# Optimization experiments

Hardware: AMD Instinct MI355X
Metric: run time of the kernel (lower is better)

The kernel has to match this reference:

```python
import jax, jax.numpy as jnp
import numpy as np

H, W = 200, 200          # detector resolution
DELX, DELY = 2.0, 2.0    # detector pixel size
EPS = 1e-8


def _rotation(theta, phi, gamma):
    # R = Rz(theta) @ Ry(phi) @ Rx(gamma), as in diffdrr's Rxyz
    ct, st = jnp.cos(theta), jnp.sin(theta)
    cp, sp = jnp.cos(phi), jnp.sin(phi)
    cg, sg = jnp.cos(gamma), jnp.sin(gamma)
    one, zero = jnp.ones_like(ct), jnp.zeros_like(ct)
    Rz = jnp.stack([jnp.stack([ct, -st, zero]), jnp.stack([st, ct, zero]), jnp.stack([zero, zero, one])])
    Ry = jnp.stack([jnp.stack([cp, zero, sp]), jnp.stack([zero, one, zero]), jnp.stack([-sp, zero, cp])])
    Rx = jnp.stack([jnp.stack([one, zero, zero]), jnp.stack([zero, cg, -sg]), jnp.stack([zero, sg, cg])])
    return Rz @ Ry @ Rx


def setup_inputs() -> dict:
    key = jax.random.key(0)
    volume = jax.random.uniform(key, (256, 256, 256), dtype=jnp.float32)
    spacing = jnp.ones((3,), dtype=jnp.float32)
    return {
        "volume": volume,
        "spacing": spacing,
        "sdr": jnp.float32(300.0),
        "theta": jnp.float32(np.pi),
        "phi": jnp.float32(0.0),
        "gamma": jnp.float32(np.pi / 2),
        "bx": jnp.float32(128.0),
        "by": jnp.float32(128.0),
        "bz": jnp.float32(128.0),
    }


def _drr_forward(volume, spacing, sdr, theta, phi, gamma, bx, by, bz):
    # DRR.__init__ flips the volume along axis 0
    vol = volume[::-1]
    nxyz = np.array(vol.shape)  # static shapes: (X, Y, Z)

    # ---- Detector.make_xrays: camera basis, source and detector plane ----
    R = sdr * _rotation(theta, phi, gamma)          # (3,3)
    source = R[:, 0]                                # rho * first column
    center = -source
    u, v = R[:, 1] / sdr, R[:, 2] / sdr             # unit in-plane basis
    t = (jnp.arange(-(H // 2), H // 2) + 1).astype(jnp.float32) * DELX
    s = (jnp.arange(-(W // 2), W // 2) + 1).astype(jnp.float32) * DELY
    trans = jnp.stack([bx, by, bz])
    src = source + trans                            # (3,)
    # cartesian_prod(t, s): row-major (t slow, s fast) -> (H*W, 3)
    tgt = (t[:, None, None] * u + s[None, :, None] * v + center + trans).reshape(H * W, 3)

    # ---- Siddon.raytrace ----
    sdd = tgt - src + EPS                           # (n, 3)
    # alpha values at every axis-aligned voxel boundary plane
    ax = (jnp.arange(nxyz[0] + 1, dtype=jnp.float32) * spacing[0] - src[0]) / sdd[:, 0:1]
    ay = (jnp.arange(nxyz[1] + 1, dtype=jnp.float32) * spacing[1] - src[1]) / sdd[:, 1:2]
    az = (jnp.arange(nxyz[2] + 1, dtype=jnp.float32) * spacing[2] - src[2]) / sdd[:, 2:3]
    alphas = jnp.concatenate([ax, ay, az], axis=-1)  # (n, P) with P = X+Y+Z+3

    # entry/exit alphas of the volume bounding box
    a0 = (0.0 - src) / sdd                           # (n, 3)
    a1 = (nxyz.astype(np.float32) * spacing - src) / sdd
    amin = jnp.max(jnp.minimum(a0, a1), axis=-1, keepdims=True)
    amax = jnp.min(jnp.maximum(a0, a1), axis=-1, keepdims=True)

    good = (alphas >= amin) & (alphas <= amax)
    alphas = jnp.sort(jnp.where(good, alphas, jnp.inf), axis=-1)  # invalid -> +inf at end

    amid = 0.5 * (alphas[:, :-1] + alphas[:, 1:])    # (n, P-1)
    step = alphas[:, 1:] - alphas[:, :-1]            # inf-inf -> nan for padding
    valid = jnp.isfinite(step)

    # midpoint positions -> voxel indices (trunc, as in torch .trunc())
    pts = src + amid[..., None] * sdd[:, None, :]    # (n, P-1, 3)
    idx = jnp.trunc(jnp.where(valid[..., None], pts, 0.0) / spacing).astype(jnp.int32)
    idx = jnp.clip(idx, 0, jnp.asarray(nxyz - 1, dtype=jnp.int32))
    vox = vol[idx[..., 0], idx[..., 1], idx[..., 2]]  # (n, P-1) gather

    drr = jnp.sum(jnp.where(valid, step, 0.0) * vox, axis=-1)  # nansum equivalent
    drr = drr * jnp.linalg.norm(tgt - src + EPS, axis=-1)       # scale by ray length
    return drr.reshape(1, 1, H, W)


def reference(volume, spacing, sdr, theta, phi, gamma, bx, by, bz):
    return _drr_forward(volume, spacing, sdr, theta, phi, gamma, bx, by, bz)
```

## Files before the change

### kernel.cpp

```cpp
#include <hip/hip_runtime.h>
#include <math.h>

#pragma clang fp contract(off)

#define SPLIT 16
static constexpr int HH = 200, WW = 200, NPL = 256;

__device__ __forceinline__ float alpha_of(float k, float sp, float src, float sdd) {
    return (k * sp - src) / sdd;
}

__global__ __launch_bounds__(256)
void drr_kernel(const float* __restrict__ vol,
                const float* __restrict__ spacing,
                const float* __restrict__ sdrP,
                const float* __restrict__ thetaP,
                const float* __restrict__ phiP,
                const float* __restrict__ gammaP,
                const float* __restrict__ bxP,
                const float* __restrict__ byP,
                const float* __restrict__ bzP,
                float* __restrict__ out)
{
    const int tid = blockIdx.x * blockDim.x + threadIdx.x;
    if (tid >= HH * WW * SPLIT) return;
    const int seg = tid / (HH * WW);
    const int rid = tid - seg * (HH * WW);
    const int it  = rid % HH;
    const int is  = rid / HH;

    const float sdr = sdrP[0];
    const float th = thetaP[0], ph = phiP[0], ga = gammaP[0];
    const float ct = cosf(th), st = sinf(th);
    const float cp = cosf(ph), sp = sinf(ph);
    const float cg = cosf(ga), sg = sinf(ga);

    const float rot[3][3] = {
        { ct*cp, ct*sp*sg - st*cg, ct*sp*cg + st*sg },
        { st*cp, st*sp*sg + ct*cg, st*sp*cg - ct*sg },
        { -sp,   cp*sg,            cp*cg            }
    };

    float source[3], u[3], v[3], trans[3];
    trans[0] = bxP[0]; trans[1] = byP[0]; trans[2] = bzP[0];
    for (int a = 0; a < 3; ++a) {
        source[a] = sdr * rot[a][0];
        u[a] = (sdr * rot[a][1]) / sdr;
        v[a] = (sdr * rot[a][2]) / sdr;
    }

    const float tc = (float)(it - HH/2 + 1) * 2.0f;
    const float sc = (float)(is - WW/2 + 1) * 2.0f;

    float src[3], sdd[3], spn[3];
    float nrm2 = 0.0f;
    for (int a = 0; a < 3; ++a) {
        spn[a] = spacing[a];
        src[a] = source[a] + trans[a];
        float tg = tc * u[a] + sc * v[a];
        tg = tg - source[a];
        tg = tg + trans[a];
        float d = (tg - src[a]) + 1e-8f;
        sdd[a] = d;
        nrm2 = nrm2 + d * d;
    }
    const bool unit = (spn[0] == 1.0f) & (spn[1] == 1.0f) & (spn[2] == 1.0f);

    float amin = -INFINITY, amax = INFINITY;
    for (int a = 0; a < 3; ++a) {
        float a0 = (0.0f - src[a]) / sdd[a];
        float a1 = (256.0f * spn[a] - src[a]) / sdd[a];
        amin = fmaxf(amin, fminf(a0, a1));
        amax = fminf(amax, fmaxf(a0, a1));
    }

    float acc = 0.0f;
    if (amax > amin) {
        const float blo = (seg == 0) ? amin
                        : amin + (amax - amin) * ((float)seg / (float)SPLIT);
        const float bhi = (seg == SPLIT - 1) ? amax
                        : amin + (amax - amin) * ((float)(seg + 1) / (float)SPLIT);

        float kf[3], kst[3], nexta[3];
        float prev = -INFINITY;

        for (int a = 0; a < 3; ++a) {
            const float sd = sdd[a], sr = src[a], spv = spn[a];
            const bool pos = sd > 0.0f;
            kst[a] = pos ? 1.0f : -1.0f;
            const float kseed = (blo * sd + sr) / spv;
            int kk;
            if (pos) {
                kk = (int)floorf(kseed) + 1;
                kk = kk < 0 ? 0 : (kk > NPL + 1 ? NPL + 1 : kk);
                while (kk > 0    && alpha_of((float)(kk-1), spv, sr, sd) >  blo) --kk;
                while (kk <= NPL && alpha_of((float)kk,     spv, sr, sd) <= blo) ++kk;
                if (kk - 1 >= 0) {
                    float ap = alpha_of((float)(kk-1), spv, sr, sd);
                    if (ap >= amin && ap > prev) prev = ap;
                }
                nexta[a] = (kk <= NPL) ? alpha_of((float)kk, spv, sr, sd) : INFINITY;
            } else {
                kk = (int)ceilf(kseed) - 1;
                kk = kk > NPL ? NPL : (kk < -1 ? -1 : kk);
                while (kk < NPL && alpha_of((float)(kk+1), spv, sr, sd) >  blo) ++kk;
                while (kk >= 0  && alpha_of((float)kk,     spv, sr, sd) <= blo) --kk;
                if (kk + 1 <= NPL) {
                    float ap = alpha_of((float)(kk+1), spv, sr, sd);
                    if (ap >= amin && ap > prev) prev = ap;
                }
                nexta[a] = (kk >= 0) ? alpha_of((float)kk, spv, sr, sd) : INFINITY;
            }
            kf[a] = (float)kk;
        }

        for (int guard = 0; guard < 1024; ++guard) {
            const float q = fminf(fminf(nexta[0], nexta[1]), nexta[2]);
            if (!(q <= bhi)) break;

            const float step = q - prev;
            const float amid = 0.5f * (prev + q);

            const float p0 = src[0] + amid * sdd[0];
            const float p1 = src[1] + amid * sdd[1];
            const float p2 = src[2] + amid * sdd[2];
            float f0, f1, f2;
            if (unit) { f0 = p0; f1 = p1; f2 = p2; }
            else      { f0 = p0 / spn[0]; f1 = p1 / spn[1]; f2 = p2 / spn[2]; }
            f0 = fminf(fmaxf(f0, 0.0f), 255.0f);
            f1 = fminf(fmaxf(f1, 0.0f), 255.0f);
            f2 = fminf(fmaxf(f2, 0.0f), 255.0f);
            const int i0 = (int)f0, i1 = (int)f1, i2 = (int)f2;

            const int addr = ((255 - i0) << 16) | (i1 << 8) | i2;
            acc = fmaf(step, vol[addr], acc);
            prev = q;

            #pragma unroll
            for (int a = 0; a < 3; ++a) {
                if (nexta[a] == q) {
                    const float nk = kf[a] + kst[a];
                    kf[a] = nk;
                    const float al = alpha_of(nk, spn[a], src[a], sdd[a]);
                    nexta[a] = (nk >= 0.0f && nk <= 256.0f) ? al : INFINITY;
                }
            }
        }
    }

    atomicAdd(&out[it * WW + is], acc * sqrtf(nrm2));
}

extern "C" void kernel_launch(void* const* d_in, const int* in_sizes, int n_in,
                              void* d_out, int out_size, void* d_ws, size_t ws_size,
                              hipStream_t stream)
{
    const float* vol     = (const float*)d_in[0];
    const float* spacing = (const float*)d_in[1];
    const float* sdr     = (const float*)d_in[2];
    const float* theta   = (const float*)d_in[3];
    const float* phi     = (const float*)d_in[4];
    const float* gamma   = (const float*)d_in[5];
    const float* bx      = (const float*)d_in[6];
    const float* by      = (const float*)d_in[7];
    const float* bz      = (const float*)d_in[8];
    float* out = (float*)d_out;

    hipMemsetAsync(out, 0, (size_t)out_size * sizeof(float), stream);

    const int threads = HH * WW * SPLIT;
    const int block   = 256;
    const int grid    = threads / block;
    drr_kernel<<<grid, block, 0, stream>>>(vol, spacing, sdr, theta, phi, gamma,
                                           bx, by, bz, out);
}
```

Baseline: 61.89 us.

## Hoist per-ray camera setup into a one-thread setup kernel, retune split and block size

Moves the rotation and trig setup out of every thread into a single-thread setup kernel that writes the camera basis to workspace; the main kernel then just loads 18 floats. Raises the per-ray segment split from 16 to 20 and halves the block size to 128 to improve load balance across segments. Adds an extra kernel launch and a dependency between the two kernels, with a fallback monolithic kernel if no workspace is available.

```diff
diff --git a/kernel.cpp b/kernel.cpp
--- a/kernel.cpp
+++ b/kernel.cpp
@@ -3,60 +3,25 @@
 
 #pragma clang fp contract(off)
 
-#define SPLIT 16
+#define SPLIT 20
 static constexpr int HH = 200, WW = 200, NPL = 256;
 
 __device__ __forceinline__ float alpha_of(float k, float sp, float src, float sdd) {
     return (k * sp - src) / sdd;
 }
 
-__global__ __launch_bounds__(256)
-void drr_kernel(const float* __restrict__ vol,
-                const float* __restrict__ spacing,
-                const float* __restrict__ sdrP,
-                const float* __restrict__ thetaP,
-                const float* __restrict__ phiP,
-                const float* __restrict__ gammaP,
-                const float* __restrict__ bxP,
-                const float* __restrict__ byP,
-                const float* __restrict__ bzP,
-                float* __restrict__ out)
-{
-    const int tid = blockIdx.x * blockDim.x + threadIdx.x;
-    if (tid >= HH * WW * SPLIT) return;
-    const int seg = tid / (HH * WW);
-    const int rid = tid - seg * (HH * WW);
-    const int it  = rid % HH;
-    const int is  = rid / HH;
-
-    const float sdr = sdrP[0];
-    const float th = thetaP[0], ph = phiP[0], ga = gammaP[0];
-    const float ct = cosf(th), st = sinf(th);
-    const float cp = cosf(ph), sp = sinf(ph);
-    const float cg = cosf(ga), sg = sinf(ga);
-
-    const float rot[3][3] = {
-        { ct*cp, ct*sp*sg - st*cg, ct*sp*cg + st*sg },
-        { st*cp, st*sp*sg + ct*cg, st*sp*cg - ct*sg },
-        { -sp,   cp*sg,            cp*cg            }
-    };
-
-    float source[3], u[3], v[3], trans[3];
-    trans[0] = bxP[0]; trans[1] = byP[0]; trans[2] = bzP[0];
-    for (int a = 0; a < 3; ++a) {
-        source[a] = sdr * rot[a][0];
-        u[a] = (sdr * rot[a][1]) / sdr;
-        v[a] = (sdr * rot[a][2]) / sdr;
-    }
-
+__device__ __forceinline__ void trace_seg(
+    const float* __restrict__ vol, float* __restrict__ out,
+    int it, int is, int seg,
+    const float u[3], const float v[3], const float source[3],
+    const float trans[3], const float src[3], const float spn[3])
+{
     const float tc = (float)(it - HH/2 + 1) * 2.0f;
     const float sc = (float)(is - WW/2 + 1) * 2.0f;
 
-    float src[3], sdd[3], spn[3];
+    float sdd[3];
     float nrm2 = 0.0f;
     for (int a = 0; a < 3; ++a) {
-        spn[a] = spacing[a];
-        src[a] = source[a] + trans[a];
         float tg = tc * u[a] + sc * v[a];
         tg = tg - source[a];
         tg = tg + trans[a];
@@ -132,7 +97,7 @@
             f2 = fminf(fmaxf(f2, 0.0f), 255.0f);
             const int i0 = (int)f0, i1 = (int)f1, i2 = (int)f2;
 
-            const int addr = ((255 - i0) << 16) | (i1 << 8) | i2;
+            const int addr = ((((255 - i0) << 8) + i1) << 8) + i2;
             acc = fmaf(step, vol[addr], acc);
             prev = q;
 
@@ -151,6 +116,104 @@
     atomicAdd(&out[it * WW + is], acc * sqrtf(nrm2));
 }
 
+__global__ void drr_setup(const float* __restrict__ spacing,
+                          const float* __restrict__ sdrP,
+                          const float* __restrict__ thetaP,
+                          const float* __restrict__ phiP,
+                          const float* __restrict__ gammaP,
+                          const float* __restrict__ bxP,
+                          const float* __restrict__ byP,
+                          const float* __restrict__ bzP,
+                          float* __restrict__ ws)
+{
+    if (threadIdx.x != 0 || blockIdx.x != 0) return;
+    const float sdr = sdrP[0];
+    const float th = thetaP[0], ph = phiP[0], ga = gammaP[0];
+    const float ct = cosf(th), st = sinf(th);
+    const float cp = cosf(ph), sp = sinf(ph);
+    const float cg = cosf(ga), sg = sinf(ga);
+
+    const float rot[3][3] = {
+        { ct*cp, ct*sp*sg - st*cg, ct*sp*cg + st*sg },
+        { st*cp, st*sp*sg + ct*cg, st*sp*cg - ct*sg },
+        { -sp,   cp*sg,            cp*cg            }
+    };
+    const float trans[3] = { bxP[0], byP[0], bzP[0] };
+    for (int a = 0; a < 3; ++a) {
+        const float source = sdr * rot[a][0];
+        ws[0  + a] = (sdr * rot[a][1]) / sdr;
+        ws[3  + a] = (sdr * rot[a][2]) / sdr;
+        ws[6  + a] = source;
+        ws[9  + a] = trans[a];
+        ws[12 + a] = source + trans[a];
+        ws[15 + a] = spacing[a];
+    }
+}
+
+__global__ __launch_bounds__(128)
+void drr_main(const float* __restrict__ vol,
+              const float* __restrict__ ws,
+              float* __restrict__ out)
+{
+    const int tid = blockIdx.x * blockDim.x + threadIdx.x;
+    const int seg = tid / (HH * WW);
+    const int rid = tid - seg * (HH * WW);
+    const int it  = rid % HH;
+    const int is  = rid / HH;
+
+    float u[3], v[3], source[3], trans[3], src[3], spn[3];
+    #pragma unroll
+    for (int a = 0; a < 3; ++a) {
+        u[a]      = ws[0  + a];
+        v[a]      = ws[3  + a];
+        source[a] = ws[6  + a];
+        trans[a]  = ws[9  + a];
+        src[a]    = ws[12 + a];
+        spn[a]    = ws[15 + a];
+    }
+    trace_seg(vol, out, it, is, seg, u, v, source, trans, src, spn);
+}
+
+__global__ __launch_bounds__(128)
+void drr_mono(const float* __restrict__ vol,
+              const float* __restrict__ spacing,
+              const float* __restrict__ sdrP,
+              const float* __restrict__ thetaP,
+              const float* __restrict__ phiP,
+              const float* __restrict__ gammaP,
+              const float* __restrict__ bxP,
+              const float* __restrict__ byP,
+              const float* __restrict__ bzP,
+              float* __restrict__ out)
+{
+    const int tid = blockIdx.x * blockDim.x + threadIdx.x;
+    const int seg = tid / (HH * WW);
+    const int rid = tid - seg * (HH * WW);
+    const int it  = rid % HH;
+    const int is  = rid / HH;
+
+    const float sdr = sdrP[0];
+    const float th = thetaP[0], ph = phiP[0], ga = gammaP[0];
+    const float ct = cosf(th), st = sinf(th);
+    const float cp = cosf(ph), sp = sinf(ph);
+    const float cg = cosf(ga), sg = sinf(ga);
+    const float rot[3][3] = {
+        { ct*cp, ct*sp*sg - st*cg, ct*sp*cg + st*sg },
+        { st*cp, st*sp*sg + ct*cg, st*sp*cg - ct*sg },
+        { -sp,   cp*sg,            cp*cg            }
+    };
+    float u[3], v[3], source[3], trans[3], src[3], spn[3];
+    trans[0] = bxP[0]; trans[1] = byP[0]; trans[2] = bzP[0];
+    for (int a = 0; a < 3; ++a) {
+        source[a] = sdr * rot[a][0];
+        u[a] = (sdr * rot[a][1]) / sdr;
+        v[a] = (sdr * rot[a][2]) / sdr;
+        src[a] = source[a] + trans[a];
+        spn[a] = spacing[a];
+    }
+    trace_seg(vol, out, it, is, seg, u, v, source, trans, src, spn);
+}
+
 extern "C" void kernel_launch(void* const* d_in, const int* in_sizes, int n_in,
                               void* d_out, int out_size, void* d_ws, size_t ws_size,
                               hipStream_t stream)
@@ -169,8 +232,15 @@
     hipMemsetAsync(out, 0, (size_t)out_size * sizeof(float), stream);
 
     const int threads = HH * WW * SPLIT;
-    const int block   = 256;
+    const int block   = 128;
     const int grid    = threads / block;
-    drr_kernel<<<grid, block, 0, stream>>>(vol, spacing, sdr, theta, phi, gamma,
-                                           bx, by, bz, out);
-}
+
+    if (ws_size >= 18 * sizeof(float)) {
+        float* ws = (float*)d_ws;
+        drr_setup<<<1, 1, 0, stream>>>(spacing, sdr, theta, phi, gamma, bx, by, bz, ws);
+        drr_main<<<grid, block, 0, stream>>>(vol, ws, out);
+    } else {
+        drr_mono<<<grid, block, 0, stream>>>(vol, spacing, sdr, theta, phi, gamma,
+                                             bx, by, bz, out);
+    }
+}
```

After: 66.70 us. 1.08x slower.

## Split ray traversal into precompute pass and dominant-axis windowed segments

Applied to the files above, without the earlier changes.

A precompute kernel now writes per-ray direction, entry and exit alphas, norm and the plane range along the dominant axis into workspace. A second kernel splits each ray into windows of 8 dominant-axis planes, so each thread walks a fixed slice of crossings. This replaces the old even split of the alpha range into 16 parts, aiming for better load balance and less per-thread setup. It adds a kernel launch and workspace traffic, and keeps the old single-kernel path as a fallback when workspace is too small.

```diff
diff --git a/kernel.cpp b/kernel.cpp
--- a/kernel.cpp
+++ b/kernel.cpp
@@ -3,31 +3,36 @@
 
 #pragma clang fp contract(off)
 
-#define SPLIT 16
-static constexpr int HH = 200, WW = 200, NPL = 256;
+static constexpr int HH = 200, WW = 200;
+static constexpr int NRAY = HH * WW;
+static constexpr int WPT  = 8;
+static constexpr int NBATCH = 33;
+
+static constexpr int WS_SDD0 = 0;
+static constexpr int WS_SDD1 = 40000;
+static constexpr int WS_SDD2 = 80000;
+static constexpr int WS_AMIN = 120000;
+static constexpr int WS_AMAX = 160000;
+static constexpr int WS_NORM = 200000;
+static constexpr int WS_KST  = 240000;
+static constexpr int WS_NK   = 280000;
+static constexpr int WS_UNI  = 320000;
+static constexpr size_t WS_BYTES = (WS_UNI + 8) * 4;
 
 __device__ __forceinline__ float alpha_of(float k, float sp, float src, float sdd) {
     return (k * sp - src) / sdd;
 }
 
 __global__ __launch_bounds__(256)
-void drr_kernel(const float* __restrict__ vol,
-                const float* __restrict__ spacing,
-                const float* __restrict__ sdrP,
-                const float* __restrict__ thetaP,
-                const float* __restrict__ phiP,
-                const float* __restrict__ gammaP,
-                const float* __restrict__ bxP,
-                const float* __restrict__ byP,
-                const float* __restrict__ bzP,
-                float* __restrict__ out)
+void drr_pre(const float* __restrict__ spacing,
+             const float* __restrict__ sdrP,  const float* __restrict__ thetaP,
+             const float* __restrict__ phiP,  const float* __restrict__ gammaP,
+             const float* __restrict__ bxP,   const float* __restrict__ byP,
+             const float* __restrict__ bzP,   float* __restrict__ ws)
 {
-    const int tid = blockIdx.x * blockDim.x + threadIdx.x;
-    if (tid >= HH * WW * SPLIT) return;
-    const int seg = tid / (HH * WW);
-    const int rid = tid - seg * (HH * WW);
-    const int it  = rid % HH;
-    const int is  = rid / HH;
+    const int rid = blockIdx.x * blockDim.x + threadIdx.x;
+    if (rid >= NRAY) return;
+    const int it = rid % HH, is = rid / HH;
 
     const float sdr = sdrP[0];
     const float th = thetaP[0], ph = phiP[0], ga = gammaP[0];
@@ -41,30 +46,29 @@
         { -sp,   cp*sg,            cp*cg            }
     };
 
-    float source[3], u[3], v[3], trans[3];
+    float u[3], v[3], source[3], trans[3], src[3], spn[3];
     trans[0] = bxP[0]; trans[1] = byP[0]; trans[2] = bzP[0];
     for (int a = 0; a < 3; ++a) {
         source[a] = sdr * rot[a][0];
         u[a] = (sdr * rot[a][1]) / sdr;
         v[a] = (sdr * rot[a][2]) / sdr;
+        src[a] = source[a] + trans[a];
+        spn[a] = spacing[a];
     }
 
     const float tc = (float)(it - HH/2 + 1) * 2.0f;
     const float sc = (float)(is - WW/2 + 1) * 2.0f;
 
-    float src[3], sdd[3], spn[3];
+    float sdd[3];
     float nrm2 = 0.0f;
     for (int a = 0; a < 3; ++a) {
-        spn[a] = spacing[a];
-        src[a] = source[a] + trans[a];
         float tg = tc * u[a] + sc * v[a];
         tg = tg - source[a];
         tg = tg + trans[a];
-        float d = (tg - src[a]) + 1e-8f;
-        sdd[a] = d;
-        nrm2 = nrm2 + d * d;
-    }
-    const bool unit = (spn[0] == 1.0f) & (spn[1] == 1.0f) & (spn[2] == 1.0f);
+        float dd = (tg - src[a]) + 1e-8f;
+        sdd[a] = dd;
+        nrm2 = nrm2 + dd * dd;
+    }
 
     float amin = -INFINITY, amax = INFINITY;
     for (int a = 0; a < 3; ++a) {
@@ -74,16 +78,264 @@
         amax = fminf(amax, fmaxf(a0, a1));
     }
 
+    ws[WS_SDD0 + rid] = sdd[0];
+    ws[WS_SDD1 + rid] = sdd[1];
+    ws[WS_SDD2 + rid] = sdd[2];
+    ws[WS_AMIN + rid] = amin;
+    ws[WS_AMAX + rid] = amax;
+    ws[WS_NORM + rid] = sqrtf(nrm2);
+
+    int* wsi = (int*)ws;
+    if (amax > amin) {
+        const float r0 = fabsf(sdd[0]) / spn[0];
+        const float r1 = fabsf(sdd[1]) / spn[1];
+        const float r2 = fabsf(sdd[2]) / spn[2];
+        int d = 0; float rb = r0;
+        if (r1 > rb) { d = 1; rb = r1; }
+        if (r2 > rb) { d = 2; }
+        const float sd = (d==0) ? sdd[0] : ((d==1) ? sdd[1] : sdd[2]);
+        const float sr = (d==0) ? src[0] : ((d==1) ? src[1] : src[2]);
+        const float spv= (d==0) ? spn[0] : ((d==1) ? spn[1] : spn[2]);
+
+        int kStart, nk;
+        if (sd > 0.0f) {
+            float kf = (amin * sd + sr) / spv;
+            int k = (int)floorf(kf); k = k < 0 ? 0 : (k > 257 ? 257 : k);
+            while (k > 0    && alpha_of((float)(k-1), spv, sr, sd) >= amin) --k;
+            while (k <= 256 && alpha_of((float)k,     spv, sr, sd) <  amin) ++k;
+            const int kA = k;
+            kf = (amax * sd + sr) / spv;
+            k = (int)floorf(kf); k = k < -1 ? -1 : (k > 256 ? 256 : k);
+            while (k < 256 && alpha_of((float)(k+1), spv, sr, sd) <= amax) ++k;
+            while (k >= 0  && alpha_of((float)k,     spv, sr, sd) >  amax) --k;
+            const int kL = k;
+            nk = kL - kA + 1; if (nk < 0) nk = 0;
+            kStart = kA;
+        } else {
+            float kf = (amin * sd + sr) / spv;
+            int k = (int)floorf(kf); k = k < -1 ? -1 : (k > 256 ? 256 : k);
+            while (k < 256 && alpha_of((float)(k+1), spv, sr, sd) >= amin) ++k;
+            while (k >= 0  && alpha_of((float)k,     spv, sr, sd) <  amin) --k;
+            const int kB = k;
+            kf = (amax * sd + sr) / spv;
+            k = (int)floorf(kf); k = k < 0 ? 0 : (k > 257 ? 257 : k);
+            while (k > 0    && alpha_of((float)(k-1), spv, sr, sd) <= amax) --k;
+            while (k <= 256 && alpha_of((float)k,     spv, sr, sd) >  amax) ++k;
+            const int kC = k;
+            nk = kB - kC + 1; if (nk < 0) nk = 0;
+            kStart = kB;
+        }
+        wsi[WS_KST + rid] = kStart;
+        wsi[WS_NK  + rid] = nk;
+    } else {
+        wsi[WS_KST + rid] = 0;
+        wsi[WS_NK  + rid] = -1;
+    }
+
+    if (rid == 0) {
+        ws[WS_UNI + 0] = src[0]; ws[WS_UNI + 1] = src[1]; ws[WS_UNI + 2] = src[2];
+        ws[WS_UNI + 3] = spn[0]; ws[WS_UNI + 4] = spn[1]; ws[WS_UNI + 5] = spn[2];
+    }
+}
+
+#define ADV_E { je += de; ne = (je >= 0 && je <= 256) ? alpha_of((float)je, sp_e, sr_e, sd_e) : INFINITY; }
+#define ADV_F { jf += df; nf = (jf >= 0 && jf <= 256) ? alpha_of((float)jf, sp_f, sr_f, sd_f) : INFINITY; }
+
+__global__ __launch_bounds__(256)
+void drr_win(const float* __restrict__ vol,
+             const float* __restrict__ ws,
+             float* __restrict__ out)
+{
+    const int rid = blockIdx.x * blockDim.x + threadIdx.x;
+    if (rid >= NRAY) return;
+    const int* __restrict__ wsi = (const int*)ws;
+    const int nk = wsi[WS_NK + rid];
+    const int w0 = blockIdx.y * WPT;
+    if (w0 > nk) return;
+
+    const float sdd0 = ws[WS_SDD0 + rid];
+    const float sdd1 = ws[WS_SDD1 + rid];
+    const float sdd2 = ws[WS_SDD2 + rid];
+    const float amin = ws[WS_AMIN + rid];
+    const float amax = ws[WS_AMAX + rid];
+    const float nrm  = ws[WS_NORM + rid];
+    const int kStart = wsi[WS_KST + rid];
+    const float src0 = ws[WS_UNI + 0], src1 = ws[WS_UNI + 1], src2 = ws[WS_UNI + 2];
+    const float spn0 = ws[WS_UNI + 3], spn1 = ws[WS_UNI + 4], spn2 = ws[WS_UNI + 5];
+    const bool unit = (spn0 == 1.0f) & (spn1 == 1.0f) & (spn2 == 1.0f);
+
+    const float r0 = fabsf(sdd0) / spn0, r1 = fabsf(sdd1) / spn1, r2 = fabsf(sdd2) / spn2;
+    int d = 0; float rb = r0;
+    if (r1 > rb) { d = 1; rb = r1; }
+    if (r2 > rb) { d = 2; }
+    const int e = (d == 0) ? 1 : 0;
+    const int f = (d == 2) ? 1 : 2;
+
+    const float sd_d = (d==0) ? sdd0 : ((d==1) ? sdd1 : sdd2);
+    const float sr_d = (d==0) ? src0 : ((d==1) ? src1 : src2);
+    const float sp_d = (d==0) ? spn0 : ((d==1) ? spn1 : spn2);
+    const float sd_e = (e==0) ? sdd0 : sdd1;
+    const float sr_e = (e==0) ? src0 : src1;
+    const float sp_e = (e==0) ? spn0 : spn1;
+    const float sd_f = (f==1) ? sdd1 : sdd2;
+    const float sr_f = (f==1) ? src1 : src2;
+    const float sp_f = (f==1) ? spn1 : spn2;
+    const int dir_d = (sd_d > 0.0f) ? 1 : -1;
+
+    float b[WPT + 1];
+    #pragma unroll
+    for (int i = 0; i <= WPT; ++i) {
+        const int m = w0 + i;
+        int km = kStart + dir_d * (m - 1);
+        km = km < 0 ? 0 : (km > 256 ? 256 : km);
+        const float av = alpha_of((float)km, sp_d, sr_d, sd_d);
+        b[i] = (m == 0) ? amin : ((m <= nk) ? av : amax);
+    }
+
+    const float LO = b[0];
+    int je, de; float ne;
+    {
+        const float sd = sd_e, sr = sr_e, spv = sp_e;
+        const bool pos = sd > 0.0f;
+        de = pos ? 1 : -1;
+        const float kf = (LO * sd + sr) / spv;
+        int j;
+        if (pos) {
+            j = (int)floorf(kf) + 1; j = j < 0 ? 0 : (j > 257 ? 257 : j);
+            while (j > 0    && alpha_of((float)(j-1), spv, sr, sd) >  LO) --j;
+            while (j <= 256 && alpha_of((float)j,     spv, sr, sd) <= LO) ++j;
+            ne = (j <= 256) ? alpha_of((float)j, spv, sr, sd) : INFINITY;
+        } else {
+            j = (int)ceilf(kf) - 1; j = j > 256 ? 256 : (j < -1 ? -1 : j);
+            while (j < 256 && alpha_of((float)(j+1), spv, sr, sd) >  LO) ++j;
+            while (j >= 0  && alpha_of((float)j,     spv, sr, sd) <= LO) --j;
+            ne = (j >= 0) ? alpha_of((float)j, spv, sr, sd) : INFINITY;
+        }
+        je = j;
+    }
+    int jf, df; float nf;
+    {
+        const float sd = sd_f, sr = sr_f, spv = sp_f;
+        const bool pos = sd > 0.0f;
+        df = pos ? 1 : -1;
+        const float kf = (LO * sd + sr) / spv;
+        int j;
+        if (pos) {
+            j = (int)floorf(kf) + 1; j = j < 0 ? 0 : (j > 257 ? 257 : j);
+            while (j > 0    && alpha_of((float)(j-1), spv, sr, sd) >  LO) --j;
+            while (j <= 256 && alpha_of((float)j,     spv, sr, sd) <= LO) ++j;
+            nf = (j <= 256) ? alpha_of((float)j, spv, sr, sd) : INFINITY;
+        } else {
+            j = (int)ceilf(kf) - 1; j = j > 256 ? 256 : (j < -1 ? -1 : j);
+            while (j < 256 && alpha_of((float)(j+1), spv, sr, sd) >  LO) ++j;
+            while (j >= 0  && alpha_of((float)j,     spv, sr, sd) <= LO) --j;
+            nf = (j >= 0) ? alpha_of((float)j, spv, sr, sd) : INFINITY;
+        }
+        jf = j;
+    }
+
+    float acc = 0.0f;
+    #pragma unroll
+    for (int i = 0; i < WPT; ++i) {
+        const int w = w0 + i;
+        if (w > nk) break;
+        const float lo = b[i], hi = b[i + 1];
+        while (ne <= lo) ADV_E;
+        while (nf <= lo) ADV_F;
+        float prev = lo;
+        for (int g = 0; g < 64; ++g) {
+            const float x = fminf(fminf(ne, nf), hi);
+            const float step = x - prev;
+            const float amid = 0.5f * (prev + x);
+
+            const float p0 = src0 + amid * sdd0;
+            const float p1 = src1 + amid * sdd1;
+            const float p2 = src2 + amid * sdd2;
+            float f0, f1v, f2v;
+            if (unit) { f0 = p0; f1v = p1; f2v = p2; }
+            else      { f0 = p0 / spn0; f1v = p1 / spn1; f2v = p2 / spn2; }
+            f0  = fminf(fmaxf(f0 , 0.0f), 255.0f);
+            f1v = fminf(fmaxf(f1v, 0.0f), 255.0f);
+            f2v = fminf(fmaxf(f2v, 0.0f), 255.0f);
+            const int i0 = (int)f0, i1 = (int)f1v, i2 = (int)f2v;
+
+            const int addr = ((((255 ^ i0) << 8) + i1) << 8) + i2;
+            acc = fmaf(step, vol[addr], acc);
+
+            if (x >= hi) break;
+            const bool ae = (ne == x), af = (nf == x);
+            if (ae) ADV_E;
+            if (af) ADV_F;
+            prev = x;
+        }
+    }
+
+    const int it = rid % HH, is = rid / HH;
+    atomicAdd(&out[it * WW + is], acc * nrm);
+}
+
+#define MSPLIT 16
+__global__ __launch_bounds__(256)
+void drr_mono(const float* __restrict__ vol,
+              const float* __restrict__ spacing,
+              const float* __restrict__ sdrP,  const float* __restrict__ thetaP,
+              const float* __restrict__ phiP,  const float* __restrict__ gammaP,
+              const float* __restrict__ bxP,   const float* __restrict__ byP,
+              const float* __restrict__ bzP,   float* __restrict__ out)
+{
+    const int tid = blockIdx.x * blockDim.x + threadIdx.x;
+    if (tid >= NRAY * MSPLIT) return;
+    const int seg = tid / NRAY;
+    const int rid = tid - seg * NRAY;
+    const int it  = rid % HH;
+    const int is  = rid / HH;
+
+    const float sdr = sdrP[0];
+    const float th = thetaP[0], ph = phiP[0], ga = gammaP[0];
+    const float ct = cosf(th), st = sinf(th);
+    const float cp = cosf(ph), sp = sinf(ph);
+    const float cg = cosf(ga), sg = sinf(ga);
+    const float rot[3][3] = {
+        { ct*cp, ct*sp*sg - st*cg, ct*sp*cg + st*sg },
+        { st*cp, st*sp*sg + ct*cg, st*sp*cg - ct*sg },
+        { -sp,   cp*sg,            cp*cg            }
+    };
+    float u[3], v[3], source[3], trans[3], src[3], spn[3];
+    trans[0] = bxP[0]; trans[1] = byP[0]; trans[2] = bzP[0];
+    for (int a = 0; a < 3; ++a) {
+        source[a] = sdr * rot[a][0];
+        u[a] = (sdr * rot[a][1]) / sdr;
+        v[a] = (sdr * rot[a][2]) / sdr;
+        src[a] = source[a] + trans[a];
+        spn[a] = spacing[a];
+    }
+    const float tc = (float)(it - HH/2 + 1) * 2.0f;
+    const float sc = (float)(is - WW/2 + 1) * 2.0f;
+    float sdd[3]; float nrm2 = 0.0f;
+    for (int a = 0; a < 3; ++a) {
+        float tg = tc * u[a] + sc * v[a];
+        tg = tg - source[a];
+        tg = tg + trans[a];
+        float dd = (tg - src[a]) + 1e-8f;
+        sdd[a] = dd;
+        nrm2 = nrm2 + dd * dd;
+    }
+    const bool unit = (spn[0] == 1.0f) & (spn[1] == 1.0f) & (spn[2] == 1.0f);
+    float amin = -INFINITY, amax = INFINITY;
+    for (int a = 0; a < 3; ++a) {
+        float a0 = (0.0f - src[a]) / sdd[a];
+        float a1 = (256.0f * spn[a] - src[a]) / sdd[a];
+        amin = fmaxf(amin, fminf(a0, a1));
+        amax = fminf(amax, fmaxf(a0, a1));
+    }
     float acc = 0.0f;
     if (amax > amin) {
         const float blo = (seg == 0) ? amin
-                        : amin + (amax - amin) * ((float)seg / (float)SPLIT);
-        const float bhi = (seg == SPLIT - 1) ? amax
-                        : amin + (amax - amin) * ((float)(seg + 1) / (float)SPLIT);
-
+                        : amin + (amax - amin) * ((float)seg / (float)MSPLIT);
+        const float bhi = (seg == MSPLIT - 1) ? amax
+                        : amin + (amax - amin) * ((float)(seg + 1) / (float)MSPLIT);
         float kf[3], kst[3], nexta[3];
         float prev = -INFINITY;
-
         for (int a = 0; a < 3; ++a) {
             const float sd = sdd[a], sr = src[a], spv = spn[a];
             const bool pos = sd > 0.0f;
@@ -92,20 +344,20 @@
             int kk;
             if (pos) {
                 kk = (int)floorf(kseed) + 1;
-                kk = kk < 0 ? 0 : (kk > NPL + 1 ? NPL + 1 : kk);
+                kk = kk < 0 ? 0 : (kk > 257 ? 257 : kk);
                 while (kk > 0    && alpha_of((float)(kk-1), spv, sr, sd) >  blo) --kk;
-                while (kk <= NPL && alpha_of((float)kk,     spv, sr, sd) <= blo) ++kk;
+                while (kk <= 256 && alpha_of((float)kk,     spv, sr, sd) <= blo) ++kk;
                 if (kk - 1 >= 0) {
                     float ap = alpha_of((float)(kk-1), spv, sr, sd);
                     if (ap >= amin && ap > prev) prev = ap;
                 }
-                nexta[a] = (kk <= NPL) ? alpha_of((float)kk, spv, sr, sd) : INFINITY;
+                nexta[a] = (kk <= 256) ? alpha_of((float)kk, spv, sr, sd) : INFINITY;
             } else {
                 kk = (int)ceilf(kseed) - 1;
-                kk = kk > NPL ? NPL : (kk < -1 ? -1 : kk);
-                while (kk < NPL && alpha_of((float)(kk+1), spv, sr, sd) >  blo) ++kk;
+                kk = kk > 256 ? 256 : (kk < -1 ? -1 : kk);
+                while (kk < 256 && alpha_of((float)(kk+1), spv, sr, sd) >  blo) ++kk;
                 while (kk >= 0  && alpha_of((float)kk,     spv, sr, sd) <= blo) --kk;
-                if (kk + 1 <= NPL) {
+                if (kk + 1 <= 256) {
                     float ap = alpha_of((float)(kk+1), spv, sr, sd);
                     if (ap >= amin && ap > prev) prev = ap;
                 }
@@ -113,14 +365,11 @@
             }
             kf[a] = (float)kk;
         }
-
         for (int guard = 0; guard < 1024; ++guard) {
             const float q = fminf(fminf(nexta[0], nexta[1]), nexta[2]);
             if (!(q <= bhi)) break;
-
             const float step = q - prev;
             const float amid = 0.5f * (prev + q);
-
             const float p0 = src[0] + amid * sdd[0];
             const float p1 = src[1] + amid * sdd[1];
             const float p2 = src[2] + amid * sdd[2];
@@ -131,23 +380,20 @@
             f1 = fminf(fmaxf(f1, 0.0f), 255.0f);
             f2 = fminf(fmaxf(f2, 0.0f), 255.0f);
             const int i0 = (int)f0, i1 = (int)f1, i2 = (int)f2;
-
-            const int addr = ((255 - i0) << 16) | (i1 << 8) | i2;
+            const int addr = ((((255 ^ i0) << 8) + i1) << 8) + i2;
             acc = fmaf(step, vol[addr], acc);
             prev = q;
-
             #pragma unroll
             for (int a = 0; a < 3; ++a) {
                 if (nexta[a] == q) {
-                    const float nk = kf[a] + kst[a];
-                    kf[a] = nk;
-                    const float al = alpha_of(nk, spn[a], src[a], sdd[a]);
-                    nexta[a] = (nk >= 0.0f && nk <= 256.0f) ? al : INFINITY;
+                    const float nkf = kf[a] + kst[a];
+                    kf[a] = nkf;
+                    const float al = alpha_of(nkf, spn[a], src[a], sdd[a]);
+                    nexta[a] = (nkf >= 0.0f && nkf <= 256.0f) ? al : INFINITY;
                 }
             }
         }
     }
-
     atomicAdd(&out[it * WW + is], acc * sqrtf(nrm2));
 }
 
@@ -168,9 +414,15 @@
 
     hipMemsetAsync(out, 0, (size_t)out_size * sizeof(float), stream);
 
-    const int threads = HH * WW * SPLIT;
-    const int block   = 256;
-    const int grid    = threads / block;
-    drr_kernel<<<grid, block, 0, stream>>>(vol, spacing, sdr, theta, phi, gamma,
-                                           bx, by, bz, out);
+    if (ws_size >= WS_BYTES) {
+        float* ws = (float*)d_ws;
+        const int rblocks = (NRAY + 255) / 256;
+        drr_pre<<<rblocks, 256, 0, stream>>>(spacing, sdr, theta, phi, gamma,
+                                             bx, by, bz, ws);
+        drr_win<<<dim3(rblocks, NBATCH), 256, 0, stream>>>(vol, ws, out);
+    } else {
+        const int threads = NRAY * MSPLIT;
+        drr_mono<<<threads / 256, 256, 0, stream>>>(vol, spacing, sdr, theta, phi,
+                                                    gamma, bx, by, bz, out);
+    }
 }
```

New measurement: 89.47 us. 44.6% more time.
